# Kernel tuning notes

Measured on AMD Instinct MI355X. Metric: run time of the kernel, lower is better.

## Reference

```python
import jax, jax.numpy as jnp
import numpy as np

EMO = 1024
FEAT = 1024
K = 128  # aggregation_k
H_LIST = (4, 8, 16)
D_LIST = tuple(EMO // h for h in H_LIST)  # (256, 128, 64)
D_SUM = sum(D_LIST)  # 448
H_SUM = sum(H_LIST)  # 28
N = len(H_LIST)      # 3 subspaces
TEMP = float(np.power(D_SUM, 0.5))


def _block_mask(sizes, total):
    m = np.zeros((len(sizes), total), np.float32)
    off = 0
    for i, s in enumerate(sizes):
        m[i, off:off + s] = 1.0
        off += s
    return jnp.asarray(m)

M_Q_BLK = _block_mask(D_LIST, D_SUM)  # [N, d_sum]
M_V_BLK = _block_mask(H_LIST, H_SUM)  # [N, h_sum]


def setup_inputs() -> dict:
    key = jax.random.key(0)
    ks = iter(jax.random.split(key, 32))
    nrm = lambda shape, s=1.0: jax.random.normal(next(ks), shape, jnp.float32) * s
    B, Lt, Lp, Nv = 32, 1024, 512, 256
    return {
        "emo_embedding": nrm((B, Lt, EMO)),
        "phr_feat": nrm((B, Lp, FEAT)),
        "video_feat": nrm((B, Nv, FEAT)),
        "w_v_W": nrm((FEAT, FEAT), FEAT ** -0.5), "w_v_b": nrm((FEAT,), 0.01),
        "agg_a_W": nrm((FEAT, K), FEAT ** -0.5), "agg_a_b": nrm((K,), 0.01),
        "agg_c_W": nrm((FEAT, EMO), FEAT ** -0.5), "agg_c_b": nrm((EMO,), 0.01),
        "ele_W": nrm((2 * EMO, 1), (2 * EMO) ** -0.5), "ele_b": nrm((1,), 0.01),
        "wq_W": nrm((EMO, D_SUM), EMO ** -0.5), "wq_b": nrm((D_SUM,), 0.01),
        "wk_W": nrm((EMO, D_SUM), EMO ** -0.5), "wk_b": nrm((D_SUM,), 0.01),
        "wv_W": nrm((EMO, H_SUM), EMO ** -0.5), "wv_b": nrm((H_SUM,), 0.01),
        "wr_W": nrm((EMO, N), EMO ** -0.5), "wr_b": nrm((N,), 0.01),
    }


def reference(emo_embedding, phr_feat, video_feat,
              w_v_W, w_v_b, agg_a_W, agg_a_b, agg_c_W, agg_c_b,
              ele_W, ele_b, wq_W, wq_b, wk_W, wk_b, wv_W, wv_b, wr_W, wr_b):
    B, Lt, _ = emo_embedding.shape
    Nv = video_feat.shape[1]
    Lp = phr_feat.shape[1]

    # --- feature_aggregation ---
    # AdaptiveAvgPool1d(Nv); Lp % Nv == 0 so it is an exact reshape-mean.
    phr = phr_feat.reshape(B, Nv, Lp // Nv, FEAT).mean(axis=2)
    combine = jnp.concatenate([phr @ w_v_W + w_v_b, video_feat], axis=1)   # [B, 2*Nv, FEAT]
    attn_a = jax.nn.softmax(combine @ agg_a_W + agg_a_b, axis=-1)          # [B, 2*Nv, K]
    agg_feat = jnp.einsum('bmk,bme->bke', attn_a, combine @ agg_c_W + agg_c_b)  # [B, K, EMO]

    # --- element_routing ---
    A_pool = jnp.einsum('ble,bke->blk', emo_embedding, agg_feat).mean(axis=1)   # [B, K]
    route = jnp.einsum('bk,bke->be', A_pool, agg_feat)[:, None, :]              # [B, 1, EMO]
    route = jnp.broadcast_to(route, emo_embedding.shape)
    R_e = jnp.tanh(jnp.concatenate([emo_embedding, route], axis=-1) @ ele_W + ele_b)  # [B, Lt, 1]
    route_emo = R_e * emo_embedding                                              # [B, Lt, EMO]

    # --- subspace_routing ---
    Q = route_emo @ wq_W + wq_b        # [B, Lt, d_sum]
    Kp = agg_feat @ wk_W + wk_b        # [B, K, d_sum]
    V = agg_feat @ wv_W + wv_b         # [B, K, h_sum]
    Rp = agg_feat @ wr_W + wr_b        # [B, K, N]

    # N masked copies of Q (block subspace masks); K/R are plain repeats, V is masked.
    Qm = (Q[:, None] * M_Q_BLK[None, :, None, :]).reshape(B, N * Lt, D_SUM)
    Kf = jnp.tile(Kp, (1, N, 1))                                         # [B, N*K, d_sum]
    Vf = (V[:, None] * M_V_BLK[None, :, None, :]).reshape(B, N * K, H_SUM)
    Rf = jnp.tile(Rp, (1, N, 1))                                         # [B, N*K, N]

    attn = jax.nn.softmax(jnp.einsum('bqd,bkd->bqk', Qm, Kf) / TEMP, axis=-1)  # [B, N*Lt, N*K]
    O = jnp.tanh(attn @ Vf).reshape(B, N, Lt, H_SUM)
    O_R = (attn @ Rf).reshape(B, N, Lt, N)

    # per-subspace head gating of route_emo
    T_list = []
    hoff = 0
    for i in range(N):
        hi, di = H_LIST[i], D_LIST[i]
        ori = route_emo.reshape(B, Lt, hi, di)
        Oi = O[:, i, :, hoff:hoff + hi][..., None]      # [B, Lt, hi, 1]
        T_list.append((ori * Oi).reshape(B, Lt, EMO))
        hoff += hi
    T = jnp.stack(T_list, axis=1)                        # [B, N, Lt, EMO]

    Rdiag = jnp.stack([O_R[:, j, :, j].mean(axis=-1) for j in range(N)], axis=1)  # [B, N]
    gate = jax.nn.softmax(Rdiag, axis=-1)[:, :, None, None]
    return emo_embedding + (gate * T).sum(axis=1)
```

## Files before the change

### kernel.cpp

```cpp
#include <hip/hip_runtime.h>
#include <math.h>

typedef long long i64;
typedef __attribute__((ext_vector_type(8))) short bf16x8;
typedef __attribute__((ext_vector_type(4))) float f32x4;

#define TEMP_ISQ 0.047245559f

__device__ __forceinline__ unsigned short f2b(float x) {
  union { float f; unsigned u; } a; a.f = x;
  return (unsigned short)((a.u + 0x7fffu + ((a.u >> 16) & 1u)) >> 16);
}
__device__ __forceinline__ float b2f(unsigned short b) {
  union { float f; unsigned u; } a; a.u = ((unsigned)b) << 16; return a.f;
}

template<int BIAS, int OUTM, int RS, int BZDIV, int XMODE = 0>
__global__ __launch_bounds__(256)
void gemm_mfma(const unsigned short* __restrict__ Ab, i64 sA,
               const unsigned short* __restrict__ Bb, i64 sB,
               const float* __restrict__ bias,
               void* __restrict__ Ob, i64 sO,
               unsigned short* __restrict__ O2b, i64 sO2,
               int Nn, int Kd, int ldA, int ldB, int ldO,
               const float* __restrict__ rowScale, i64 sRS,
               const float* __restrict__ rsAdd)
{
  __shared__ unsigned short As[8192];
  __shared__ unsigned short Bs[8192];
  const int tid = threadIdx.x;
  const int w = tid >> 6, lane = tid & 63;

  const int gx = gridDim.x, gy = gridDim.y;
  int nwg = gx * gy * gridDim.z;
  int bid = blockIdx.x + gx * (blockIdx.y + gy * blockIdx.z);
  int L = bid;
  if ((nwg & 7) == 0) L = (bid & 7) * (nwg >> 3) + (bid >> 3);
  const int bx = L % gx;
  int rem = L / gx;
  const int by = rem % gy;
  const int z  = rem / gy;

  const int m0 = by * 128, n0 = bx * 128;
  const unsigned short* A;
  const unsigned short* B;
  int KdL = Kd;
  if (XMODE == 1) {
    int bb = z / 3, ii = z - bb * 3;
    const int dof_[3] = {0, 256, 384};
    const int kdt_[3] = {256, 128, 64};
    A = Ab + dof_[ii] + (i64)bb * sA;
    B = Bb + dof_[ii] + (i64)bb * sB;
    KdL = kdt_[ii];
  } else {
    A = Ab + (i64)z * sA;
    B = Bb + (i64)(BZDIV == 1 ? z : z / BZDIV) * sB;
  }
  const int wr = w >> 1, wc = w & 1;
  const int rS = tid >> 3, sS = tid & 7;
  const int cL = lane & 15, sl = lane >> 4;

  f32x4 acc[4][4];
  #pragma unroll
  for (int i = 0; i < 4; ++i)
    #pragma unroll
    for (int j = 0; j < 4; ++j) acc[i][j] = (f32x4){0.f, 0.f, 0.f, 0.f};

  for (int k0 = 0; k0 < KdL; k0 += 64) {
    #pragma unroll
    for (int q = 0; q < 4; ++q) {
      int r = rS + q * 32;
      int sg = sS ^ (r & 7);
      const unsigned short* sa = A + (i64)(m0 + r) * ldA + k0 + sg * 8;
      const unsigned short* sb = B + (i64)(n0 + r) * ldB + k0 + sg * 8;
      __builtin_amdgcn_global_load_lds(
          (__attribute__((address_space(1))) void*)sa,
          (__attribute__((address_space(3))) void*)&As[r * 64 + sS * 8], 16, 0, 0);
      __builtin_amdgcn_global_load_lds(
          (__attribute__((address_space(1))) void*)sb,
          (__attribute__((address_space(3))) void*)&Bs[r * 64 + sS * 8], 16, 0, 0);
    }
    __syncthreads();
    bf16x8 af[2][4], bfv[2][4];
    #pragma unroll
    for (int kk = 0; kk < 2; ++kk) {
      #pragma unroll
      for (int mi = 0; mi < 4; ++mi) {
        int rr = wr * 64 + mi * 16 + cL;
        int ph = (kk * 4 + sl) ^ (rr & 7);
        af[kk][mi] = *(const bf16x8*)&As[rr * 64 + ph * 8];
      }
      #pragma unroll
      for (int ni = 0; ni < 4; ++ni) {
        int rr = wc * 64 + ni * 16 + cL;
        int ph = (kk * 4 + sl) ^ (rr & 7);
        bfv[kk][ni] = *(const bf16x8*)&Bs[rr * 64 + ph * 8];
      }
    }
    #pragma unroll
    for (int kk = 0; kk < 2; ++kk)
      #pragma unroll
      for (int mi = 0; mi < 4; ++mi)
        #pragma unroll
        for (int ni = 0; ni < 4; ++ni)
          acc[mi][ni] = __builtin_amdgcn_mfma_f32_16x16x32_bf16(af[kk][mi], bfv[kk][ni], acc[mi][ni], 0, 0, 0);
    __syncthreads();
  }

  #pragma unroll
  for (int mi = 0; mi < 4; ++mi) {
    const int rowb = m0 + wr * 64 + mi * 16 + sl * 4;
    #pragma unroll
    for (int ni = 0; ni < 4; ++ni) {
      const int col = n0 + wc * 64 + ni * 16 + cL;
      if (col < Nn) {
        float bc = (BIAS == 1) ? bias[col] : 0.f;
        #pragma unroll
        for (int rg = 0; rg < 4; ++rg) {
          float v = acc[mi][ni][rg];
          if (RS) v *= tanhf(rowScale[(i64)z * sRS + rowb + rg] + rsAdd[z]);
          v += bc;
          if (BIAS == 2) v += bias[rowb + rg];
          i64 oidx = (i64)(rowb + rg) * ldO + col;
          if (OUTM == 0)      ((float*)Ob)[(i64)z * sO + oidx] = v;
          else if (OUTM == 1) ((unsigned short*)Ob)[(i64)z * sO + oidx] = f2b(v);
          else if (OUTM == 3) ((float*)Ob)[(i64)z * sO + oidx] = tanhf(v * (1.f / 3.f));
          else {
            ((float*)Ob)[(i64)z * sO + oidx] = v;
            O2b[(i64)z * sO2 + oidx] = f2b(v);
          }
        }
      }
    }
  }
}

__global__ __launch_bounds__(256)
void emo_pass1(const float* __restrict__ emo, const float* __restrict__ eleW,
               unsigned short* __restrict__ emoB, float* __restrict__ colPart,
               float* __restrict__ dotE) {
  int b = blockIdx.y, lc = blockIdx.x;
  int t = threadIdx.x, lane = t & 63, w = t >> 6;
  float4 w4 = ((const float4*)eleW)[t];
  float4 acc = make_float4(0.f, 0.f, 0.f, 0.f);
  __shared__ float dw[16][4];
  const float4* src = (const float4*)emo + ((i64)b * 1024 + lc * 16) * 256;
  ushort4* dst = (ushort4*)emoB + ((i64)b * 1024 + lc * 16) * 256;
  #pragma unroll 4
  for (int lr = 0; lr < 16; ++lr) {
    float4 v = src[lr * 256 + t];
    acc.x += v.x; acc.y += v.y; acc.z += v.z; acc.w += v.w;
    float d = v.x * w4.x + v.y * w4.y + v.z * w4.z + v.w * w4.w;
    #pragma unroll
    for (int o = 32; o; o >>= 1) d += __shfl_xor(d, o);
    if (!lane) dw[lr][w] = d;
    ushort4 o4; o4.x = f2b(v.x); o4.y = f2b(v.y); o4.z = f2b(v.z); o4.w = f2b(v.w);
    dst[lr * 256 + t] = o4;
  }
  __syncthreads();
  if (t < 16) dotE[(i64)b * 1024 + lc * 16 + t] = dw[t][0] + dw[t][1] + dw[t][2] + dw[t][3];
  ((float4*)colPart)[((i64)b * 64 + lc) * 256 + t] = acc;
}

__global__ void colmean2(const float* __restrict__ colPart, float* __restrict__ emomean) {
  int b = blockIdx.y, e = blockIdx.x * 256 + threadIdx.x;
  float s = 0.f;
  #pragma unroll 8
  for (int lc = 0; lc < 64; ++lc) s += colPart[((i64)b * 64 + lc) * 1024 + e];
  emomean[b * 1024 + e] = s * (1.f / 1024.f);
}

__global__ __launch_bounds__(256)
void transpose_all(const float* __restrict__ w_v_W, const float* __restrict__ agg_a_W,
                   const float* __restrict__ agg_c_W, const float* __restrict__ wq_W,
                   const float* __restrict__ wk_W, const float* __restrict__ wv_W,
                   const float* __restrict__ wr_W,
                   unsigned short* __restrict__ wvT, unsigned short* __restrict__ aaT,
                   unsigned short* __restrict__ acT, unsigned short* __restrict__ wqT,
                   unsigned short* __restrict__ kvrT) {
  __shared__ float T[32][33];
  int bx = blockIdx.x;
  const float* in; unsigned short* out; int N, Npad, s0;
  if (bx < 32)      { in = w_v_W;   out = wvT;                     N = 1024; Npad = 1024; s0 = 0; }
  else if (bx < 36) { in = agg_a_W; out = aaT;                     N = 128;  Npad = 128;  s0 = 32; }
  else if (bx < 68) { in = agg_c_W; out = acT;                     N = 1024; Npad = 1024; s0 = 36; }
  else if (bx < 84) { in = wq_W;    out = wqT;                     N = 448;  Npad = 512;  s0 = 68; }
  else if (bx < 98) { in = wk_W;    out = kvrT;                    N = 448;  Npad = 448;  s0 = 84; }
  else if (bx < 99) { in = wv_W;    out = kvrT + (i64)448 * 1024;  N = 28;   Npad = 28;   s0 = 98; }
  else              { in = wr_W;    out = kvrT + (i64)476 * 1024;  N = 3;    Npad = 36;   s0 = 99; }
  int n0 = (bx - s0) * 32, k0 = blockIdx.y * 32;
  int t = threadIdx.x;
  #pragma unroll
  for (int p = 0; p < 4; ++p) {
    int idx = t + 256 * p; int kk = idx >> 5, nn = idx & 31;
    float v = 0.f;
    if (n0 + nn < N) v = in[(i64)(k0 + kk) * N + (n0 + nn)];
    T[nn][kk] = v;
  }
  __syncthreads();
  #pragma unroll
  for (int p = 0; p < 4; ++p) {
    int idx = t + 256 * p; int nn = idx >> 5, kk = idx & 31;
    if (n0 + nn < Npad) out[(i64)(n0 + nn) * 1024 + (k0 + kk)] = f2b(T[nn][kk]);
  }
}

__global__ void kvr_bias_kernel(const float* wkb, const float* wvb, const float* wrb, float* out) {
  int t = blockIdx.x * 256 + threadIdx.x;
  if (t >= 480) return;
  out[t] = (t < 448) ? wkb[t] : (t < 476) ? wvb[t - 448] : (t < 479) ? wrb[t - 476] : 0.f;
}

__global__ void pool_phr(const float* __restrict__ phr, unsigned short* __restrict__ out) {
  i64 idx = (i64)blockIdx.x * 256 + threadIdx.x;
  if (idx >= 2097152) return;
  i64 bm = idx >> 8; int c = (int)(idx & 255);
  i64 b = bm >> 8, m = bm & 255;
  const float4* r0 = (const float4*)(phr + (b * 512 + 2 * m) * 1024) + c;
  const float4* r1 = (const float4*)(phr + (b * 512 + 2 * m + 1) * 1024) + c;
  float4 a = *r0, d = *r1;
  ushort4 o;
  o.x = f2b(0.5f * (a.x + d.x)); o.y = f2b(0.5f * (a.y + d.y));
  o.z = f2b(0.5f * (a.z + d.z)); o.w = f2b(0.5f * (a.w + d.w));
  ((ushort4*)out)[idx] = o;
}

__global__ void vconv(const float* __restrict__ video, unsigned short* __restrict__ combine) {
  i64 idx = (i64)blockIdx.x * 256 + threadIdx.x;
  if (idx >= 2097152) return;
  i64 b = idx >> 16, r = idx & 65535;
  float4 v = ((const float4*)video)[idx];
  ushort4 o;
  o.x = f2b(v.x); o.y = f2b(v.y); o.z = f2b(v.z); o.w = f2b(v.w);
  ((ushort4*)combine)[b * 131072 + 65536 + r] = o;
}

__global__ void vt_fill(const unsigned short* __restrict__ KVR, unsigned short* __restrict__ VT) {
  int b = blockIdx.y;
  int idx = blockIdx.x * 256 + threadIdx.x;
  int n = idx >> 7, k = idx & 127;
  unsigned short v = 0;
  if (n < 28) v = KVR[(i64)b * 61440 + k * 480 + 448 + n];
  VT[((i64)b * 128 + n) * 128 + k] = v;
}

__global__ void softmax_attn_a(const float* __restrict__ logits, unsigned short* __restrict__ outT) {
  int gw = (int)(((i64)blockIdx.x * blockDim.x + threadIdx.x) >> 6);
  int lane = threadIdx.x & 63;
  if (gw >= 32 * 512) return;
  int b = gw >> 9, m = gw & 511;
  const float* p = logits + (i64)gw * 128;
  float x0 = p[lane], x1 = p[lane + 64];
  float mx = fmaxf(x0, x1);
  #pragma unroll
  for (int o = 32; o; o >>= 1) mx = fmaxf(mx, __shfl_xor(mx, o));
  float e0 = expf(x0 - mx), e1 = expf(x1 - mx);
  float s = e0 + e1;
  #pragma unroll
  for (int o = 32; o; o >>= 1) s += __shfl_xor(s, o);
  float inv = 1.f / s;
  unsigned short* o0 = outT + (i64)b * 128 * 512 + m;
  o0[(i64)lane * 512] = f2b(e0 * inv);
  o0[(i64)(lane + 64) * 512] = f2b(e1 * inv);
}

__global__ void softmax_P_bf(const unsigned short* __restrict__ PL, unsigned short* __restrict__ P) {
  i64 gw = ((i64)blockIdx.x * blockDim.x + threadIdx.x) >> 6;
  int lane = threadIdx.x & 63;
  if (gw >= 98304) return;
  const unsigned short* p = PL + gw * 128;
  float x0 = b2f(p[lane]) * TEMP_ISQ, x1 = b2f(p[lane + 64]) * TEMP_ISQ;
  float mx = fmaxf(x0, x1);
  #pragma unroll
  for (int o = 32; o; o >>= 1) mx = fmaxf(mx, __shfl_xor(mx, o));
  float e0 = expf(x0 - mx), e1 = expf(x1 - mx);
  float s = e0 + e1;
  #pragma unroll
  for (int o = 32; o; o >>= 1) s += __shfl_xor(s, o);
  float inv = 1.f / s;
  P[gw * 128 + lane] = f2b(e0 * inv);
  P[gw * 128 + lane + 64] = f2b(e1 * inv);
}

__global__ void apool_kernel(const float* __restrict__ emomean, const float* __restrict__ agg,
                             float* __restrict__ Apool) {
  int gw = (int)(((i64)blockIdx.x * blockDim.x + threadIdx.x) >> 6);
  int lane = threadIdx.x & 63;
  if (gw >= 32 * 128) return;
  int b = gw >> 7, k = gw & 127;
  const float* ag = agg + ((i64)b * 128 + k) * 1024;
  const float* em = emomean + (i64)b * 1024;
  float s = 0.f;
  #pragma unroll
  for (int j = 0; j < 16; ++j) { int e = j * 64 + lane; s += em[e] * ag[e]; }
  #pragma unroll
  for (int o = 32; o; o >>= 1) s += __shfl_down(s, o);
  if (!lane) Apool[gw] = s;
}

__global__ void route_kernel(const float* __restrict__ Apool, const float* __restrict__ agg,
                             float* __restrict__ route) {
  int b = blockIdx.y;
  int e = blockIdx.x * 256 + threadIdx.x;
  __shared__ float Ap[128];
  if (threadIdx.x < 128) Ap[threadIdx.x] = Apool[b * 128 + threadIdx.x];
  __syncthreads();
  const float* ag = agg + (i64)b * 128 * 1024 + e;
  float s = 0.f;
  #pragma unroll 8
  for (int k = 0; k < 128; ++k) s += Ap[k] * ag[(i64)k * 1024];
  route[b * 1024 + e] = s;
}

__global__ void rb_kernel(const float* __restrict__ route, const float* __restrict__ eleW,
                          const float* __restrict__ eleb, float* __restrict__ rb) {
  int b = blockIdx.x, t = threadIdx.x;
  float s = 0.f;
  for (int j = t; j < 1024; j += 256) s += route[b * 1024 + j] * eleW[1024 + j];
  __shared__ float red[256];
  red[t] = s; __syncthreads();
  for (int o = 128; o > 0; o >>= 1) { if (t < o) red[t] += red[t + o]; __syncthreads(); }
  if (t == 0) rb[b] = red[0] + eleb[0];
}

__global__ void pmean1_kernel(const unsigned short* __restrict__ P, float* __restrict__ Ppart) {
  int bi = blockIdx.x, c = blockIdx.y, k = threadIdx.x;
  const unsigned short* p = P + ((i64)bi * 1024 + c * 128) * 128 + k;
  float s = 0.f;
  for (int l = 0; l < 128; ++l) s += b2f(p[(i64)l * 128]);
  Ppart[((i64)bi * 8 + c) * 128 + k] = s;
}

__global__ void pmean2_rdiag(const float* __restrict__ Ppart, const unsigned short* __restrict__ KVR,
                             float* __restrict__ gate) {
  int b = blockIdx.x, t = threadIdx.x;
  __shared__ float red[128];
  __shared__ float rd[3];
  for (int i = 0; i < 3; ++i) {
    float s = 0.f;
    #pragma unroll
    for (int c = 0; c < 8; ++c) s += Ppart[((i64)(b * 3 + i) * 8 + c) * 128 + t];
    float v = s * (1.f / 1024.f) * b2f(KVR[(i64)b * 61440 + t * 480 + 476 + i]);
    red[t] = v; __syncthreads();
    for (int o = 64; o > 0; o >>= 1) { if (t < o) red[t] += red[t + o]; __syncthreads(); }
    if (t == 0) rd[i] = red[0];
    __syncthreads();
  }
  if (t == 0) {
    float m = fmaxf(rd[0], fmaxf(rd[1], rd[2]));
    float e0 = expf(rd[0] - m), e1 = expf(rd[1] - m), e2 = expf(rd[2] - m);
    float inv = 1.f / (e0 + e1 + e2);
    gate[b * 3 + 0] = e0 * inv; gate[b * 3 + 1] = e1 * inv; gate[b * 3 + 2] = e2 * inv;
  }
}

__global__ __launch_bounds__(256)
void final_kernel(const unsigned short* __restrict__ emoB, const float* __restrict__ dotE,
                  const float* __restrict__ rbv, const float* __restrict__ O,
                  const float* __restrict__ gate, float* __restrict__ out) {
  i64 bl = blockIdx.x;
  int b = (int)(bl >> 10), l = (int)(bl & 1023);
  __shared__ float Gg[16];
  int t = threadIdx.x;
  if (t < 16) {
    float g0 = gate[b * 3], g1 = gate[b * 3 + 1], g2 = gate[b * 3 + 2];
    float o0 = O[((i64)(b * 3 + 0) * 1024 + l) * 28 + (t >> 2)];
    float o1 = O[((i64)(b * 3 + 1) * 1024 + l) * 28 + 4 + (t >> 1)];
    float o2 = O[((i64)(b * 3 + 2) * 1024 + l) * 28 + 12 + t];
    Gg[t] = g0 * o0 + g1 * o1 + g2 * o2;
  }
  __syncthreads();
  float re = tanhf(dotE[bl] + rbv[b]);
  ushort4 e4 = ((const ushort4*)(emoB + bl * 1024))[t];
  float g = 1.f + re * Gg[t >> 4];
  ((float4*)(out + bl * 1024))[t] =
      make_float4(b2f(e4.x) * g, b2f(e4.y) * g, b2f(e4.z) * g, b2f(e4.w) * g);
}

extern "C" void kernel_launch(void* const* d_in, const int* in_sizes, int n_in,
                              void* d_out, int out_size, void* d_ws, size_t ws_size,
                              hipStream_t stream) {
  const float* emo     = (const float*)d_in[0];
  const float* phr     = (const float*)d_in[1];
  const float* video   = (const float*)d_in[2];
  const float* w_v_W   = (const float*)d_in[3];
  const float* w_v_b   = (const float*)d_in[4];
  const float* agg_a_W = (const float*)d_in[5];
  const float* agg_a_b = (const float*)d_in[6];
  const float* agg_c_W = (const float*)d_in[7];
  const float* agg_c_b = (const float*)d_in[8];
  const float* ele_W   = (const float*)d_in[9];
  const float* ele_b   = (const float*)d_in[10];
  const float* wq_W    = (const float*)d_in[11];
  const float* wq_b    = (const float*)d_in[12];
  const float* wk_W    = (const float*)d_in[13];
  const float* wk_b    = (const float*)d_in[14];
  const float* wv_W    = (const float*)d_in[15];
  const float* wv_b    = (const float*)d_in[16];
  const float* wr_W    = (const float*)d_in[17];
  const float* wr_b    = (const float*)d_in[18];

  char* ws = (char*)d_ws;
  const i64 oEmoB    = 0;
  const i64 oCombine = 67108864;
  const i64 oPL      = 67108864;
  const i64 oPooled  = 100663296;
  const i64 oLogitsA = 100663296;
  const i64 oAggF    = 100663296;
  const i64 oO       = 100663296;
  const i64 oCT      = 117440512;
  const i64 oQ       = 117440512;
  const i64 oAttnAT  = 150994944;
  const i64 oAggB    = 155189248;
  const i64 oWvT     = 163577856;
  const i64 oAaT     = 165675008;
  const i64 oAcT     = 165937152;
  const i64 oWqT     = 168034304;
  const i64 oKvrT    = 169082880;
  const i64 oKVR     = 170131456;
  const i64 oVT      = 174063616;
  const i64 oKvrB    = 175112192;
  const i64 oEmomean = 175116288;
  const i64 oColPart = 175247360;
  const i64 oDotE    = 183635968;
  const i64 oApool   = 183767040;
  const i64 oRoute   = 183783424;
  const i64 oRb      = 183914496;
  const i64 oPpart   = 183914752;
  const i64 oGate    = 184307968;

  unsigned short* emoB    = (unsigned short*)(ws + oEmoB);
  unsigned short* combine = (unsigned short*)(ws + oCombine);
  unsigned short* PL      = (unsigned short*)(ws + oPL);
  unsigned short* P       = PL;
  unsigned short* pooled  = (unsigned short*)(ws + oPooled);
  float*          logitsA = (float*)(ws + oLogitsA);
  float*          aggF    = (float*)(ws + oAggF);
  float*          O       = (float*)(ws + oO);
  unsigned short* CT      = (unsigned short*)(ws + oCT);
  unsigned short* Q       = (unsigned short*)(ws + oQ);
  unsigned short* attnAT  = (unsigned short*)(ws + oAttnAT);
  unsigned short* aggB    = (unsigned short*)(ws + oAggB);
  unsigned short* wvT     = (unsigned short*)(ws + oWvT);
  unsigned short* aaT     = (unsigned short*)(ws + oAaT);
  unsigned short* acT     = (unsigned short*)(ws + oAcT);
  unsigned short* wqT     = (unsigned short*)(ws + oWqT);
  unsigned short* kvrT    = (unsigned short*)(ws + oKvrT);
  unsigned short* KVR     = (unsigned short*)(ws + oKVR);
  unsigned short* VT      = (unsigned short*)(ws + oVT);
  float*          kvrB    = (float*)(ws + oKvrB);
  float*          emomean = (float*)(ws + oEmomean);
  float*          colPart = (float*)(ws + oColPart);
  float*          dotE    = (float*)(ws + oDotE);
  float*          Apool   = (float*)(ws + oApool);
  float*          route   = (float*)(ws + oRoute);
  float*          rbv     = (float*)(ws + oRb);
  float*          Ppart   = (float*)(ws + oPpart);
  float*          gate    = (float*)(ws + oGate);

  dim3 blk(256);

  emo_pass1<<<dim3(64, 32), blk, 0, stream>>>(emo, ele_W, emoB, colPart, dotE);

  transpose_all<<<dim3(101, 32), blk, 0, stream>>>(w_v_W, agg_a_W, agg_c_W, wq_W, wk_W, wv_W, wr_W,
                                                   wvT, aaT, acT, wqT, kvrT);
  kvr_bias_kernel<<<2, blk, 0, stream>>>(wk_b, wv_b, wr_b, kvrB);

  pool_phr<<<8192, blk, 0, stream>>>(phr, pooled);
  vconv<<<8192, blk, 0, stream>>>(video, combine);
  gemm_mfma<1, 1, 0, 1><<<dim3(8, 2, 32), blk, 0, stream>>>(pooled, 262144, wvT, 0, w_v_b,
      (void*)combine, 524288, nullptr, 0, 1024, 1024, 1024, 1024, 1024, nullptr, 0, nullptr);
  gemm_mfma<1, 0, 0, 1><<<dim3(1, 4, 32), blk, 0, stream>>>(combine, 524288, aaT, 0, agg_a_b,
      (void*)logitsA, 65536, nullptr, 0, 128, 1024, 1024, 1024, 128, nullptr, 0, nullptr);
  softmax_attn_a<<<4096, blk, 0, stream>>>(logitsA, attnAT);
  gemm_mfma<2, 1, 0, 1><<<dim3(4, 8, 32), blk, 0, stream>>>(acT, 0, combine, 524288, agg_c_b,
      (void*)CT, 524288, nullptr, 0, 512, 1024, 1024, 1024, 512, nullptr, 0, nullptr);
  gemm_mfma<0, 2, 0, 1><<<dim3(8, 1, 32), blk, 0, stream>>>(attnAT, 65536, CT, 524288, nullptr,
      (void*)aggF, 131072, aggB, 131072, 1024, 512, 512, 512, 1024, nullptr, 0, nullptr);

  colmean2<<<dim3(4, 32), blk, 0, stream>>>(colPart, emomean);
  apool_kernel<<<1024, blk, 0, stream>>>(emomean, aggF, Apool);
  route_kernel<<<dim3(4, 32), blk, 0, stream>>>(Apool, aggF, route);
  rb_kernel<<<32, blk, 0, stream>>>(route, ele_W, ele_b, rbv);

  gemm_mfma<1, 1, 0, 1><<<dim3(4, 1, 32), blk, 0, stream>>>(aggB, 131072, kvrT, 0, kvrB,
      (void*)KVR, 61440, nullptr, 0, 480, 1024, 1024, 1024, 480, nullptr, 0, nullptr);
  vt_fill<<<dim3(64, 32), blk, 0, stream>>>(KVR, VT);
  gemm_mfma<1, 1, 1, 1><<<dim3(4, 8, 32), blk, 0, stream>>>(emoB, 1048576, wqT, 0, wq_b,
      (void*)Q, 458752, nullptr, 0, 448, 1024, 1024, 1024, 448, dotE, 1024, rbv);

  gemm_mfma<0, 1, 0, 1, 1><<<dim3(1, 8, 96), blk, 0, stream>>>(Q, 458752, KVR, 61440, nullptr,
      (void*)PL, 131072, nullptr, 0, 128, 0, 448, 480, 128, nullptr, 0, nullptr);

  softmax_P_bf<<<24576, blk, 0, stream>>>(PL, P);
  pmean1_kernel<<<dim3(96, 8), 128, 0, stream>>>(P, Ppart);
  gemm_mfma<0, 3, 0, 3><<<dim3(1, 8, 96), blk, 0, stream>>>(P, 131072, VT, 16384, nullptr,
      (void*)O, 28672, nullptr, 0, 28, 128, 128, 128, 28, nullptr, 0, nullptr);
  pmean2_rdiag<<<32, 128, 0, stream>>>(Ppart, KVR, gate);
  final_kernel<<<32768, blk, 0, stream>>>(emoB, dotE, rbv, O, gate, (float*)d_out);
}
```

Before: 453.0 us.

## Double-buffer GEMM LDS tiles with K-step of 32 to overlap loads

The MFMA GEMM now splits LDS into two buffers of half the K-depth (32 instead of 64). It issues the global-to-LDS load for the next tile before computing on the current one, with one barrier per iteration. The goal is to hide global load latency behind MFMA work. In exchange it halves the work per barrier and narrows the XOR swizzle to 4 segments, which may raise bank conflicts and sync overhead. The next-tile loads are asynchronous and only the end-of-iteration barrier protects them, so there is a risk the data is not complete when read.

```diff
diff --git a/kernel.cpp b/kernel.cpp
--- a/kernel.cpp
+++ b/kernel.cpp
@@ -26,8 +26,8 @@
                const float* __restrict__ rowScale, i64 sRS,
                const float* __restrict__ rsAdd)
 {
-  __shared__ unsigned short As[8192];
-  __shared__ unsigned short Bs[8192];
+  __shared__ unsigned short As[2][4096];
+  __shared__ unsigned short Bs[2][4096];
   const int tid = threadIdx.x;
   const int w = tid >> 6, lane = tid & 63;
 
@@ -57,7 +57,7 @@
     B = Bb + (i64)(BZDIV == 1 ? z : z / BZDIV) * sB;
   }
   const int wr = w >> 1, wc = w & 1;
-  const int rS = tid >> 3, sS = tid & 7;
+  const int rS = tid >> 2, sS = tid & 3;
   const int cL = lane & 15, sl = lane >> 4;
 
   f32x4 acc[4][4];
@@ -66,44 +66,46 @@
     #pragma unroll
     for (int j = 0; j < 4; ++j) acc[i][j] = (f32x4){0.f, 0.f, 0.f, 0.f};
 
-  for (int k0 = 0; k0 < KdL; k0 += 64) {
-    #pragma unroll
-    for (int q = 0; q < 4; ++q) {
-      int r = rS + q * 32;
-      int sg = sS ^ (r & 7);
+  auto STAGE = [&](int buf, int k0) {
+    #pragma unroll
+    for (int q = 0; q < 2; ++q) {
+      int r = rS + q * 64;
+      int sg = sS ^ (r & 3);
       const unsigned short* sa = A + (i64)(m0 + r) * ldA + k0 + sg * 8;
       const unsigned short* sb = B + (i64)(n0 + r) * ldB + k0 + sg * 8;
       __builtin_amdgcn_global_load_lds(
           (__attribute__((address_space(1))) void*)sa,
-          (__attribute__((address_space(3))) void*)&As[r * 64 + sS * 8], 16, 0, 0);
+          (__attribute__((address_space(3))) void*)&As[buf][r * 32 + sS * 8], 16, 0, 0);
       __builtin_amdgcn_global_load_lds(
           (__attribute__((address_space(1))) void*)sb,
-          (__attribute__((address_space(3))) void*)&Bs[r * 64 + sS * 8], 16, 0, 0);
+          (__attribute__((address_space(3))) void*)&Bs[buf][r * 32 + sS * 8], 16, 0, 0);
     }
-    __syncthreads();
-    bf16x8 af[2][4], bfv[2][4];
-    #pragma unroll
-    for (int kk = 0; kk < 2; ++kk) {
+  };
+
+  STAGE(0, 0);
+  __syncthreads();
+
+  for (int k0 = 0; k0 < KdL; k0 += 32) {
+    const int cur = (k0 >> 5) & 1;
+    if (k0 + 32 < KdL) STAGE(cur ^ 1, k0 + 32);
+    bf16x8 af[4], bfv[4];
+    #pragma unroll
+    for (int mi = 0; mi < 4; ++mi) {
+      int rr = wr * 64 + mi * 16 + cL;
+      int ph = sl ^ (rr & 3);
+      af[mi] = *(const bf16x8*)&As[cur][rr * 32 + ph * 8];
+    }
+    #pragma unroll
+    for (int ni = 0; ni < 4; ++ni) {
+      int rr = wc * 64 + ni * 16 + cL;
+      int ph = sl ^ (rr & 3);
+      bfv[ni] = *(const bf16x8*)&Bs[cur][rr * 32 + ph * 8];
+    }
+    #pragma unroll
+    for (int mi = 0; mi < 4; ++mi)
       #pragma unroll
-      for (int mi = 0; mi < 4; ++mi) {
-        int rr = wr * 64 + mi * 16 + cL;
-        int ph = (kk * 4 + sl) ^ (rr & 7);
-        af[kk][mi] = *(const bf16x8*)&As[rr * 64 + ph * 8];
-      }
-      #pragma unroll
-      for (int ni = 0; ni < 4; ++ni) {
-        int rr = wc * 64 + ni * 16 + cL;
-        int ph = (kk * 4 + sl) ^ (rr & 7);
-        bfv[kk][ni] = *(const bf16x8*)&Bs[rr * 64 + ph * 8];
-      }
-    }
-    #pragma unroll
-    for (int kk = 0; kk < 2; ++kk)
-      #pragma unroll
-      for (int mi = 0; mi < 4; ++mi)
-        #pragma unroll
-        for (int ni = 0; ni < 4; ++ni)
-          acc[mi][ni] = __builtin_amdgcn_mfma_f32_16x16x32_bf16(af[kk][mi], bfv[kk][ni], acc[mi][ni], 0, 0, 0);
+      for (int ni = 0; ni < 4; ++ni)
+        acc[mi][ni] = __builtin_amdgcn_mfma_f32_16x16x32_bf16(af[mi], bfv[ni], acc[mi][ni], 0, 0, 0);
     __syncthreads();
   }
 
```

Result: no change. 460.4 us (+1.6%).
